# Kernel tuning notes

Measured on AMD Instinct MI355X. Metric: run time of the kernel, lower is better.

The kernel has to match this reference:

```python
import jax, jax.numpy as jnp
import numpy as np

H = 12          # num_heads
LENS_T = 64     # template tokens
LENS_S = 256    # search tokens
KEEP = int(0.7 * LENS_S)  # 179 kept search tokens


def _ln(x, s, b):
    mu = jnp.mean(x, axis=-1, keepdims=True)
    var = jnp.mean(jnp.square(x - mu), axis=-1, keepdims=True)
    return (x - mu) / jnp.sqrt(var + 1e-5) * s + b


def setup_inputs() -> dict:
    key = jax.random.key(0)
    ks = jax.random.split(key, 8)
    B, C, Hh = 32, 768, 3072
    N = LENS_T + LENS_S
    w = lambda k, shape: jax.random.normal(k, shape, jnp.float32) * 0.02
    return {
        "x": jax.random.normal(ks[0], (B, N, C), jnp.float32),
        "global_index_t": jnp.tile(jnp.arange(LENS_T, dtype=jnp.int32), (B, 1)),
        "global_index_s": jnp.tile(jnp.arange(LENS_S, dtype=jnp.int32), (B, 1)),
        "norm1_s": jnp.ones((C,), jnp.float32), "norm1_b": jnp.zeros((C,), jnp.float32),
        "qkv_w": w(ks[1], (C, 3 * C)), "qkv_b": jnp.zeros((3 * C,), jnp.float32),
        "proj_w": w(ks[2], (C, C)), "proj_b": jnp.zeros((C,), jnp.float32),
        "norm2_s": jnp.ones((C,), jnp.float32), "norm2_b": jnp.zeros((C,), jnp.float32),
        "fc1_w": w(ks[3], (C, Hh)), "fc1_b": jnp.zeros((Hh,), jnp.float32),
        "fc2_w": w(ks[4], (Hh, C)), "fc2_b": jnp.zeros((C,), jnp.float32),
        "gcn_w": w(ks[5], (C, C)), "gcn_b": jnp.zeros((C,), jnp.float32),
        "norm3_s": jnp.ones((C,), jnp.float32), "norm3_b": jnp.zeros((C,), jnp.float32),
    }


def reference(x, global_index_t, global_index_s,
              norm1_s, norm1_b, qkv_w, qkv_b, proj_w, proj_b,
              norm2_s, norm2_b, fc1_w, fc1_b, fc2_w, fc2_b,
              gcn_w, gcn_b, norm3_s, norm3_b):
    B, N, C = x.shape
    hd = C // H
    scale = hd ** -0.5

    # --- attention (attn weights explicitly materialized) ---
    h = _ln(x, norm1_s, norm1_b)
    qkv = (h @ qkv_w + qkv_b).reshape(B, N, 3, H, hd).transpose(2, 0, 3, 1, 4)
    q, k, v = qkv[0], qkv[1], qkv[2]                      # [B,H,N,hd]
    attn = jax.nn.softmax(jnp.einsum('bhqd,bhkd->bhqk', q, k) * scale, axis=-1)
    xa = jnp.einsum('bhqk,bhkd->bhqd', attn, v).transpose(0, 2, 1, 3).reshape(B, N, C)
    xa = xa @ proj_w + proj_b
    x = x + xa

    # --- MLP ---
    x_res = x
    h2 = _ln(x, norm2_s, norm2_b)
    h2 = jax.nn.gelu(h2 @ fc1_w + fc1_b, approximate=False) @ fc2_w + fc2_b
    x = x_res + h2

    # --- GCN using template<->search attention as adjacency ---
    # adjacency = [[0, w_ts], [w_ts^T, 0]]; exploit block sparsity instead of
    # materializing the dense [B,N,N] matrix.
    w_ts = jnp.sum(attn[:, :, :LENS_T, LENS_T:], axis=1) / H   # [B,T,S]
    w_ts = jax.nn.softmax(w_ts, axis=2)
    support = x @ gcn_w + gcn_b
    out_t = jnp.einsum('bts,bsd->btd', w_ts, support[:, LENS_T:])   # top block
    out_s = jnp.einsum('bts,btd->bsd', w_ts, support[:, :LENS_T])   # bottom block
    x = jnp.concatenate([out_t, out_s], axis=1)
    x = x + _ln(x, norm3_s, norm3_b)

    # --- top-k token pruning on search tokens ---
    score_s = jnp.mean(attn[:, :, :LENS_T, LENS_T:], axis=(1, 2))   # [B,S]
    order = jnp.argsort(-score_s, axis=1)
    keep_indices = order[:, :KEEP]
    removed_index_s = order[:, KEEP:]
    gs_new = jnp.take_along_axis(global_index_s, keep_indices, axis=1)
    idx = jnp.concatenate([global_index_t.astype(jnp.int32), keep_indices + LENS_T], axis=1)
    x = jnp.take_along_axis(x, jnp.broadcast_to(idx[..., None], (B, idx.shape[1], C)), axis=1)
    return (x, global_index_t, gs_new, removed_index_s, attn)
```

## Files before the change

### kernel.cpp

```cpp
#include <hip/hip_runtime.h>
#include <math.h>

#define NKEEP 179
#define NREM  77
#define NOUT_ROWS 243

typedef __bf16 bf16x8 __attribute__((ext_vector_type(8)));
typedef float f32x4 __attribute__((ext_vector_type(4)));

__device__ __forceinline__ unsigned short f2bf(float f) {
  unsigned u = __builtin_bit_cast(unsigned, f);
  u = (u + 0x7FFFu + ((u >> 16) & 1u)) >> 16;
  return (unsigned short)u;
}

__device__ __forceinline__ void gload_lds16(const void* g, void* l) {
  __builtin_amdgcn_global_load_lds((const __attribute__((address_space(1))) void*)g,
                                   (__attribute__((address_space(3))) void*)l,
                                   16, 0, 0);
}

template<int RESID, int OUTMODE>
__global__ __launch_bounds__(256)
void ln_kernel(const float* __restrict__ in, const float* __restrict__ gs,
               const float* __restrict__ gb, void* __restrict__ outp,
               void* __restrict__ outp2) {
  int row = blockIdx.x;
  const float* p = in + (size_t)row * 768;
  int tid = threadIdx.x;
  float v0 = p[tid], v1 = p[tid + 256], v2 = p[tid + 512];
  __shared__ double rs[256], rq[256];
  double d0 = v0, d1 = v1, d2 = v2;
  rs[tid] = d0 + d1 + d2;
  rq[tid] = d0 * d0 + d1 * d1 + d2 * d2;
  __syncthreads();
  for (int st = 128; st > 0; st >>= 1) {
    if (tid < st) { rs[tid] += rs[tid + st]; rq[tid] += rq[tid + st]; }
    __syncthreads();
  }
  double mu  = rs[0] * (1.0 / 768.0);
  double var = rq[0] * (1.0 / 768.0) - mu * mu;
  float rstd = (float)rsqrt(var + 1e-5);
  float muf = (float)mu;
  float y0 = (v0 - muf) * rstd * gs[tid]       + gb[tid];
  float y1 = (v1 - muf) * rstd * gs[tid + 256] + gb[tid + 256];
  float y2 = (v2 - muf) * rstd * gs[tid + 512] + gb[tid + 512];
  if (RESID) { y0 += v0; y1 += v1; y2 += v2; }
  if (OUTMODE == 0 || OUTMODE == 2) {
    float* o = (float*)outp + (size_t)row * 768;
    o[tid] = y0; o[tid + 256] = y1; o[tid + 512] = y2;
  }
  if (OUTMODE == 1) {
    unsigned short* o = (unsigned short*)outp + (size_t)row * 768;
    o[tid] = f2bf(y0); o[tid + 256] = f2bf(y1); o[tid + 512] = f2bf(y2);
  }
  if (OUTMODE == 2) {
    unsigned short* o = (unsigned short*)outp2 + (size_t)row * 768;
    o[tid] = f2bf(y0); o[tid + 256] = f2bf(y1); o[tid + 512] = f2bf(y2);
  }
}

__global__ __launch_bounds__(256)
void wtrans_kernel(const float* __restrict__ W, unsigned short* __restrict__ Wt,
                   int K, int N) {
  __shared__ float t[32][33];
  int n0 = blockIdx.x * 32, k0 = blockIdx.y * 32;
  int tid = threadIdx.x;
#pragma unroll
  for (int p = 0; p < 4; p++) {
    int idx = tid + p * 256;
    int r = idx >> 5, c = idx & 31;
    t[r][c] = W[(size_t)(k0 + r) * N + n0 + c];
  }
  __syncthreads();
#pragma unroll
  for (int p = 0; p < 4; p++) {
    int idx = tid + p * 256;
    int r = idx >> 5, c = idx & 31;
    Wt[(size_t)(n0 + r) * K + k0 + c] = f2bf(t[c][r]);
  }
}

template<int ACT, int RES, int OUTBF>
__global__ __launch_bounds__(256)
void gemm_bf16_kernel(const unsigned short* __restrict__ A,
                      const unsigned short* __restrict__ Bt,
                      const float* __restrict__ bias, const float* __restrict__ res,
                      void* __restrict__ outp, int M, int K, int N) {
  __shared__ unsigned short Al[128 * 64];
  __shared__ unsigned short Bl[128 * 64];
  int tid = threadIdx.x;
  int lane = tid & 63, wid = tid >> 6;
  int wr = wid >> 1, wc = wid & 1;
  int bm0 = blockIdx.x * 128, bn0 = blockIdx.y * 128;

  int r8 = lane >> 3;
  int csw = lane & 7;
  int csrc = csw ^ r8;

  const unsigned short* Abase = A + (size_t)bm0 * K + (size_t)csrc * 8;
  const unsigned short* Bbase = Bt + (size_t)bn0 * K + (size_t)csrc * 8;

  f32x4 acc[4][4] = {};

  int mrow = lane & 15;
  int kch = lane >> 4;
  int key = mrow & 7;

  for (int k0 = 0; k0 < K; k0 += 64) {
#pragma unroll
    for (int i = 0; i < 4; i++) {
      int rr = wid * 32 + i * 8;
      gload_lds16(Abase + (size_t)(rr + r8) * K + k0, Al + rr * 64);
      gload_lds16(Bbase + (size_t)(rr + r8) * K + k0, Bl + rr * 64);
    }
    __syncthreads();
#pragma unroll
    for (int ks = 0; ks < 2; ks++) {
      bf16x8 af[4], bfr[4];
#pragma unroll
      for (int f = 0; f < 4; f++) {
        int ra = wr * 64 + f * 16 + mrow;
        int ca = (ks * 4 + kch) ^ key;
        af[f] = *reinterpret_cast<const bf16x8*>(&Al[ra * 64 + ca * 8]);
        int rb = wc * 64 + f * 16 + mrow;
        bfr[f] = *reinterpret_cast<const bf16x8*>(&Bl[rb * 64 + ca * 8]);
      }
#pragma unroll
      for (int fm = 0; fm < 4; fm++)
#pragma unroll
        for (int fn = 0; fn < 4; fn++)
          acc[fm][fn] = __builtin_amdgcn_mfma_f32_16x16x32_bf16(
              af[fm], bfr[fn], acc[fm][fn], 0, 0, 0);
    }
    __syncthreads();
  }
#pragma unroll
  for (int fm = 0; fm < 4; fm++) {
#pragma unroll
    for (int j = 0; j < 4; j++) {
      int row = bm0 + wr * 64 + fm * 16 + (lane >> 4) * 4 + j;
#pragma unroll
      for (int fn = 0; fn < 4; fn++) {
        int col = bn0 + wc * 64 + fn * 16 + (lane & 15);
        float c = acc[fm][fn][j] + bias[col];
        if (ACT == 1) c = 0.5f * c * (1.0f + erff(c * 0.70710678118654752f));
        if (RES) c += res[(size_t)row * N + col];
        if (OUTBF) ((unsigned short*)outp)[(size_t)row * N + col] = f2bf(c);
        else       ((float*)outp)[(size_t)row * N + col] = c;
      }
    }
  }
}

__global__ __launch_bounds__(256)
void gemm_qkv_bf16_kernel(const unsigned short* __restrict__ A,
                          const unsigned short* __restrict__ Bt,
                          const float* __restrict__ bias,
                          float* __restrict__ Qb, float* __restrict__ Vb) {
  __shared__ unsigned short Al[128 * 64];
  __shared__ unsigned short Bl[128 * 64];
  const int K = 768;
  int tid = threadIdx.x;
  int lane = tid & 63, wid = tid >> 6;
  int wr = wid >> 1, wc = wid & 1;
  int by = blockIdx.y;
  int colbase = (by < 6) ? by * 128 : (by - 6) * 128 + 1536;
  int bm0 = blockIdx.x * 128;

  int r8 = lane >> 3;
  int csw = lane & 7;
  int csrc = csw ^ r8;

  const unsigned short* Abase = A + (size_t)bm0 * K + (size_t)csrc * 8;
  const unsigned short* Bbase = Bt + (size_t)colbase * K + (size_t)csrc * 8;

  f32x4 acc[4][4] = {};
  int mrow = lane & 15;
  int kch = lane >> 4;
  int key = mrow & 7;

  for (int k0 = 0; k0 < K; k0 += 64) {
#pragma unroll
    for (int i = 0; i < 4; i++) {
      int rr = wid * 32 + i * 8;
      gload_lds16(Abase + (size_t)(rr + r8) * K + k0, Al + rr * 64);
      gload_lds16(Bbase + (size_t)(rr + r8) * K + k0, Bl + rr * 64);
    }
    __syncthreads();
#pragma unroll
    for (int ks = 0; ks < 2; ks++) {
      bf16x8 af[4], bfr[4];
#pragma unroll
      for (int f = 0; f < 4; f++) {
        int ra = wr * 64 + f * 16 + mrow;
        int ca = (ks * 4 + kch) ^ key;
        af[f] = *reinterpret_cast<const bf16x8*>(&Al[ra * 64 + ca * 8]);
        int rb = wc * 64 + f * 16 + mrow;
        bfr[f] = *reinterpret_cast<const bf16x8*>(&Bl[rb * 64 + ca * 8]);
      }
#pragma unroll
      for (int fm = 0; fm < 4; fm++)
#pragma unroll
        for (int fn = 0; fn < 4; fn++)
          acc[fm][fn] = __builtin_amdgcn_mfma_f32_16x16x32_bf16(
              af[fm], bfr[fn], acc[fm][fn], 0, 0, 0);
    }
    __syncthreads();
  }
#pragma unroll
  for (int fm = 0; fm < 4; fm++) {
#pragma unroll
    for (int j = 0; j < 4; j++) {
      int row = bm0 + wr * 64 + fm * 16 + (lane >> 4) * 4 + j;
      int b = row / 320, nr = row - b * 320;
#pragma unroll
      for (int fn = 0; fn < 4; fn++) {
        int col = colbase + wc * 64 + fn * 16 + (lane & 15);
        int sel = col / 768;
        int rem = col - sel * 768;
        int h = rem >> 6, d = rem & 63;
        float* dstb = (sel == 0) ? Qb : Vb;
        dstb[(((size_t)(b * 12 + h) * 320 + nr) << 6) + d] = acc[fm][fn][j] + bias[col];
      }
    }
  }
}

template<int ROWMAP>
__global__ __launch_bounds__(256)
void gemm_prec_kernel(const float* __restrict__ A, const float* __restrict__ W,
                      const float* __restrict__ bias, int colOff,
                      float* __restrict__ Dst) {
  __shared__ float AsT[32][68];
  __shared__ float Bs[32][68];
  int tid = threadIdx.x;
  int tx = tid & 15, ty = tid >> 4;
  int bm0 = blockIdx.x * 64, bn0 = blockIdx.y * 64;

  int arow[2];
#pragma unroll
  for (int q = 0; q < 2; q++) {
    int idx = tid + q * 256;
    int m = bm0 + (idx >> 3);
    arow[q] = ROWMAP ? ((m >> 6) * 320 + (m & 63)) : m;
  }
  const float* Wbase = W + colOff + bn0;

  double master[4][4] = {};
  for (int k0 = 0; k0 < 768; k0 += 32) {
    float4 av[2], bv[2];
#pragma unroll
    for (int q = 0; q < 2; q++) {
      int idx = tid + q * 256;
      av[q] = *(const float4*)(A + (size_t)arow[q] * 768 + k0 + (idx & 7) * 4);
      int br = idx >> 4, bc4 = idx & 15;
      bv[q] = *(const float4*)(Wbase + (size_t)(k0 + br) * 2304 + bc4 * 4);
    }
    __syncthreads();
#pragma unroll
    for (int q = 0; q < 2; q++) {
      int idx = tid + q * 256;
      int r = idx >> 3, kc8 = idx & 7;
      AsT[kc8 * 4 + 0][r] = av[q].x;
      AsT[kc8 * 4 + 1][r] = av[q].y;
      AsT[kc8 * 4 + 2][r] = av[q].z;
      AsT[kc8 * 4 + 3][r] = av[q].w;
      *(float4*)&Bs[idx >> 4][(idx & 15) * 4] = bv[q];
    }
    __syncthreads();
#pragma unroll
    for (int half = 0; half < 2; half++) {
      float chunk[4][4] = {};
#pragma unroll
      for (int kk = 0; kk < 16; kk++) {
        int kkk = half * 16 + kk;
        float a[4], bb[4];
        *(float4*)a  = *(const float4*)&AsT[kkk][ty * 4];
        *(float4*)bb = *(const float4*)&Bs[kkk][tx * 4];
#pragma unroll
        for (int i = 0; i < 4; i++)
#pragma unroll
          for (int j = 0; j < 4; j++) chunk[i][j] = fmaf(a[i], bb[j], chunk[i][j]);
      }
#pragma unroll
      for (int i = 0; i < 4; i++)
#pragma unroll
        for (int j = 0; j < 4; j++) master[i][j] += (double)chunk[i][j];
    }
    __syncthreads();
  }
  int n0 = bn0 + tx * 4;
  int h = n0 >> 6, d = n0 & 63;
#pragma unroll
  for (int i = 0; i < 4; i++) {
    int m = bm0 + ty * 4 + i;
    int b, nr;
    if (ROWMAP) { b = m >> 6; nr = m & 63; }
    else        { b = m / 320; nr = m - b * 320; }
    float* dst = Dst + (((size_t)(b * 12 + h) * 320 + nr) << 6) + d;
    float4 v;
    v.x = (float)master[i][0] + bias[colOff + n0];
    v.y = (float)master[i][1] + bias[colOff + n0 + 1];
    v.z = (float)master[i][2] + bias[colOff + n0 + 2];
    v.w = (float)master[i][3] + bias[colOff + n0 + 3];
    *(float4*)dst = v;
  }
}

__global__ __launch_bounds__(256)
void attn_fused_kernel(const float* __restrict__ Qb, const float* __restrict__ Kb,
                       const float* __restrict__ Vb, float* __restrict__ attn,
                       unsigned short* __restrict__ xa) {
  __shared__ float Qs[64][68];
  __shared__ float Ks[64][68];
  float (*Ps)[68] = Qs;
  int bid = blockIdx.x;
  int qt = bid / 384, bh = bid % 384;
  int h = bh % 12, b = bh / 12;
  int q0 = qt * 64;
  int t = threadIdx.x;
  int tx = t & 15, ty = t >> 4;
  const float* Qg = Qb + (((size_t)bh * 320 + q0) << 6);
  const float* Kg = Kb + (((size_t)bh * 320) << 6);
  const float* Vg = Vb + (((size_t)bh * 320) << 6);
  float* attn_bh = attn + ((size_t)bh * 320 + q0) * 320;

  {
    int r = t >> 2, c = (t & 3) * 16;
    const float* src = Qg + (r << 6) + c;
#pragma unroll
    for (int i = 0; i < 4; i++)
      *(float4*)&Qs[r][c + i * 4] = *(const float4*)(src + i * 4);
  }

  float s[4][20];
  float mrow[4] = {-1e30f, -1e30f, -1e30f, -1e30f};

#pragma unroll
  for (int kc = 0; kc < 5; ++kc) {
    __syncthreads();
    {
      int r = t >> 2, c = (t & 3) * 16;
      const float* src = Kg + ((size_t)(kc * 64 + r) << 6) + c;
#pragma unroll
      for (int i = 0; i < 4; i++)
        *(float4*)&Ks[r][c + i * 4] = *(const float4*)(src + i * 4);
    }
    __syncthreads();
    float acc[4][4] = {};
#pragma unroll 4
    for (int d0 = 0; d0 < 64; d0 += 4) {
      float4 qv[4], kv[4];
#pragma unroll
      for (int i = 0; i < 4; i++) qv[i] = *(const float4*)&Qs[ty * 4 + i][d0];
#pragma unroll
      for (int j = 0; j < 4; j++) kv[j] = *(const float4*)&Ks[tx * 4 + j][d0];
#pragma unroll
      for (int i = 0; i < 4; i++)
#pragma unroll
        for (int j = 0; j < 4; j++) {
          acc[i][j] = fmaf(qv[i].x, kv[j].x, acc[i][j]);
          acc[i][j] = fmaf(qv[i].y, kv[j].y, acc[i][j]);
          acc[i][j] = fmaf(qv[i].z, kv[j].z, acc[i][j]);
          acc[i][j] = fmaf(qv[i].w, kv[j].w, acc[i][j]);
        }
    }
#pragma unroll
    for (int i = 0; i < 4; i++) {
      float sx = acc[i][0] * 0.125f, sy = acc[i][1] * 0.125f;
      float sz = acc[i][2] * 0.125f, sw = acc[i][3] * 0.125f;
      mrow[i] = fmaxf(mrow[i], fmaxf(fmaxf(sx, sy), fmaxf(sz, sw)));
      s[i][kc * 4 + 0] = sx; s[i][kc * 4 + 1] = sy;
      s[i][kc * 4 + 2] = sz; s[i][kc * 4 + 3] = sw;
    }
  }
#pragma unroll
  for (int i = 0; i < 4; i++) {
    mrow[i] = fmaxf(mrow[i], __shfl_xor(mrow[i], 1, 16));
    mrow[i] = fmaxf(mrow[i], __shfl_xor(mrow[i], 2, 16));
    mrow[i] = fmaxf(mrow[i], __shfl_xor(mrow[i], 4, 16));
    mrow[i] = fmaxf(mrow[i], __shfl_xor(mrow[i], 8, 16));
  }

  double lsum[4] = {0.0, 0.0, 0.0, 0.0};
#pragma unroll
  for (int i = 0; i < 4; i++)
#pragma unroll
    for (int c = 0; c < 20; c++) {
      float e = expf(s[i][c] - mrow[i]);
      s[i][c] = e;
      lsum[i] += (double)e;
    }
#pragma unroll
  for (int i = 0; i < 4; i++) {
    lsum[i] += __shfl_xor(lsum[i], 1, 16);
    lsum[i] += __shfl_xor(lsum[i], 2, 16);
    lsum[i] += __shfl_xor(lsum[i], 4, 16);
    lsum[i] += __shfl_xor(lsum[i], 8, 16);
  }
  float inv[4];
#pragma unroll
  for (int i = 0; i < 4; i++) inv[i] = (float)(1.0 / lsum[i]);

#pragma unroll
  for (int i = 0; i < 4; i++)
#pragma unroll
    for (int kc = 0; kc < 5; kc++) {
      float4 sv;
      sv.x = s[i][kc * 4 + 0] * inv[i];
      sv.y = s[i][kc * 4 + 1] * inv[i];
      sv.z = s[i][kc * 4 + 2] * inv[i];
      sv.w = s[i][kc * 4 + 3] * inv[i];
      *(float4*)&attn_bh[(size_t)(ty * 4 + i) * 320 + kc * 64 + tx * 4] = sv;
    }

  float acc2[4][4] = {};
  for (int kc = 0; kc < 5; ++kc) {
    __syncthreads();
    {
      int r = t >> 2, c = (t & 3) * 16;
      const float* src = Vg + ((size_t)(kc * 64 + r) << 6) + c;
#pragma unroll
      for (int i = 0; i < 4; i++)
        *(float4*)&Ks[r][c + i * 4] = *(const float4*)(src + i * 4);
    }
#pragma unroll
    for (int i = 0; i < 4; i++) {
      float4 sv;
      sv.x = s[i][kc * 4 + 0] * inv[i];
      sv.y = s[i][kc * 4 + 1] * inv[i];
      sv.z = s[i][kc * 4 + 2] * inv[i];
      sv.w = s[i][kc * 4 + 3] * inv[i];
      *(float4*)&Ps[ty * 4 + i][tx * 4] = sv;
    }
    __syncthreads();
#pragma unroll 4
    for (int kk4 = 0; kk4 < 16; ++kk4) {
      float4 pv[4], vv[4];
#pragma unroll
      for (int i = 0; i < 4; i++)
        pv[i] = *(const float4*)&Ps[ty * 4 + i][kk4 * 4];
#pragma unroll
      for (int l = 0; l < 4; l++) vv[l] = *(const float4*)&Ks[kk4 * 4 + l][tx * 4];
#pragma unroll
      for (int i = 0; i < 4; i++) {
        acc2[i][0] = fmaf(pv[i].x, vv[0].x, acc2[i][0]);
        acc2[i][1] = fmaf(pv[i].x, vv[0].y, acc2[i][1]);
        acc2[i][2] = fmaf(pv[i].x, vv[0].z, acc2[i][2]);
        acc2[i][3] = fmaf(pv[i].x, vv[0].w, acc2[i][3]);
        acc2[i][0] = fmaf(pv[i].y, vv[1].x, acc2[i][0]);
        acc2[i][1] = fmaf(pv[i].y, vv[1].y, acc2[i][1]);
        acc2[i][2] = fmaf(pv[i].y, vv[1].z, acc2[i][2]);
        acc2[i][3] = fmaf(pv[i].y, vv[1].w, acc2[i][3]);
        acc2[i][0] = fmaf(pv[i].z, vv[2].x, acc2[i][0]);
        acc2[i][1] = fmaf(pv[i].z, vv[2].y, acc2[i][1]);
        acc2[i][2] = fmaf(pv[i].z, vv[2].z, acc2[i][2]);
        acc2[i][3] = fmaf(pv[i].z, vv[2].w, acc2[i][3]);
        acc2[i][0] = fmaf(pv[i].w, vv[3].x, acc2[i][0]);
        acc2[i][1] = fmaf(pv[i].w, vv[3].y, acc2[i][1]);
        acc2[i][2] = fmaf(pv[i].w, vv[3].z, acc2[i][2]);
        acc2[i][3] = fmaf(pv[i].w, vv[3].w, acc2[i][3]);
      }
    }
  }
#pragma unroll
  for (int i = 0; i < 4; i++) {
    unsigned short* dst = xa + (size_t)(b * 320 + q0 + ty * 4 + i) * 768 + h * 64 + tx * 4;
    uint2 pk;
    pk.x = (unsigned)f2bf(acc2[i][0]) | ((unsigned)f2bf(acc2[i][1]) << 16);
    pk.y = (unsigned)f2bf(acc2[i][2]) | ((unsigned)f2bf(acc2[i][3]) << 16);
    *(uint2*)dst = pk;
  }
}

__global__ __launch_bounds__(256)
void wts_kernel(const float* __restrict__ attn, float* __restrict__ wts) {
  int bid = blockIdx.x;
  int tt = bid & 63, b = bid >> 6;
  int s = threadIdx.x;
  float acc = 0.0f;
  const float* base = attn + (((size_t)(b * 12)) * 320 + tt) * 320 + 64 + s;
#pragma unroll
  for (int h = 0; h < 12; h++) acc += base[(size_t)h * 320 * 320];
  acc *= (1.0f / 12.0f);
  __shared__ float red[256];
  red[s] = acc; __syncthreads();
  for (int st = 128; st > 0; st >>= 1) {
    if (s < st) red[s] = fmaxf(red[s], red[s + st]);
    __syncthreads();
  }
  float m = red[0]; __syncthreads();
  float e = expf(acc - m);
  red[s] = e; __syncthreads();
  for (int st = 128; st > 0; st >>= 1) {
    if (s < st) red[s] += red[s + st];
    __syncthreads();
  }
  wts[(size_t)bid * 256 + s] = e / red[0];
}

__global__ __launch_bounds__(256)
void out_t_kernel(const float* __restrict__ wts, const float* __restrict__ sup,
                  float* __restrict__ x3) {
  int idx = blockIdx.x * 256 + threadIdx.x;
  int c = idx % 768;
  int tt = (idx / 768) % 64;
  int b = idx / (768 * 64);
  const float* wrow = wts + (size_t)(b * 64 + tt) * 256;
  const float* sp = sup + ((size_t)(b * 320 + 64)) * 768 + c;
  float acc = 0.0f;
  for (int s = 0; s < 256; s++) acc = fmaf(wrow[s], sp[(size_t)s * 768], acc);
  x3[((size_t)(b * 320 + tt)) * 768 + c] = acc;
}

__global__ __launch_bounds__(256)
void out_s_kernel(const float* __restrict__ wts, const float* __restrict__ sup,
                  float* __restrict__ x3) {
  int idx = blockIdx.x * 256 + threadIdx.x;
  int c = idx % 768;
  int s = (idx / 768) % 256;
  int b = idx / (768 * 256);
  const float* wp = wts + (size_t)(b * 64) * 256 + s;
  const float* sp = sup + ((size_t)(b * 320)) * 768 + c;
  float acc = 0.0f;
#pragma unroll 4
  for (int tt = 0; tt < 64; tt++) acc = fmaf(wp[(size_t)tt * 256], sp[(size_t)tt * 768], acc);
  x3[((size_t)(b * 320 + 64 + s)) * 768 + c] = acc;
}

__global__ __launch_bounds__(256)
void score_part_kernel(const float* __restrict__ attn, double* __restrict__ part) {
  int h = blockIdx.x, b = blockIdx.y;
  int s = threadIdx.x;
  const float* base = attn + (((size_t)(b * 12 + h)) * 320) * 320 + 64 + s;
  double acc = 0.0;
  for (int tt = 0; tt < 64; tt++) acc += (double)base[(size_t)tt * 320];
  part[((size_t)(b * 12 + h)) * 256 + s] = acc;
}

__global__ __launch_bounds__(256)
void score_final_kernel(const double* __restrict__ part, const int* __restrict__ git,
                        const int* __restrict__ gis, int* __restrict__ order_ws,
                        float* __restrict__ out_git, float* __restrict__ out_gs,
                        float* __restrict__ out_rm) {
  int b = blockIdx.x, s = threadIdx.x;
  double acc = 0.0;
#pragma unroll
  for (int h = 0; h < 12; h++) acc += part[((size_t)(b * 12 + h)) * 256 + s];
  __shared__ double sc[256];
  __shared__ int ord[256];
  sc[s] = acc;
  __syncthreads();
  double my = sc[s];
  int r = 0;
  for (int i = 0; i < 256; i++) {
    double si = sc[i];
    r += (si > my) || (si == my && i < s);
  }
  ord[r] = s;
  __syncthreads();
  int o = ord[s];
  order_ws[b * 256 + s] = o;
  if (s < NKEEP) out_gs[b * NKEEP + s] = (float)gis[b * 256 + o];
  else           out_rm[b * NREM + (s - NKEEP)] = (float)o;
  if (s < 64)    out_git[b * 64 + s] = (float)git[b * 64 + s];
}

__global__ __launch_bounds__(256)
void gather_kernel(const float* __restrict__ x3, const int* __restrict__ git,
                   const int* __restrict__ order_ws, float* __restrict__ out) {
  int bid = blockIdx.x;
  int j = bid % NOUT_ROWS, b = bid / NOUT_ROWS;
  int src = (j < 64) ? git[b * 64 + j] : (order_ws[b * 256 + (j - 64)] + 64);
  const float* p = x3 + ((size_t)(b * 320 + src)) * 768;
  float* o = out + ((size_t)(b * NOUT_ROWS + j)) * 768;
  int tid = threadIdx.x;
  o[tid] = p[tid]; o[tid + 256] = p[tid + 256]; o[tid + 512] = p[tid + 512];
}

extern "C" void kernel_launch(void* const* d_in, const int* in_sizes, int n_in,
                              void* d_out, int out_size, void* d_ws, size_t ws_size,
                              hipStream_t stream) {
  (void)in_sizes; (void)n_in; (void)out_size; (void)ws_size;
  const float* x      = (const float*)d_in[0];
  const int*   git    = (const int*)d_in[1];
  const int*   gis    = (const int*)d_in[2];
  const float* n1s    = (const float*)d_in[3];
  const float* n1b    = (const float*)d_in[4];
  const float* qkv_w  = (const float*)d_in[5];
  const float* qkv_b  = (const float*)d_in[6];
  const float* proj_w = (const float*)d_in[7];
  const float* proj_b = (const float*)d_in[8];
  const float* n2s    = (const float*)d_in[9];
  const float* n2b    = (const float*)d_in[10];
  const float* fc1_w  = (const float*)d_in[11];
  const float* fc1_b  = (const float*)d_in[12];
  const float* fc2_w  = (const float*)d_in[13];
  const float* fc2_b  = (const float*)d_in[14];
  const float* gcn_w  = (const float*)d_in[15];
  const float* gcn_b  = (const float*)d_in[16];
  const float* n3s    = (const float*)d_in[17];
  const float* n3b    = (const float*)d_in[18];

  float* out     = (float*)d_out;
  float* out_x   = out;
  float* out_git = out + 5971968;
  float* out_gs  = out + 5974016;
  float* out_rm  = out + 5979744;
  float* attn    = out + 5982208;

  float* w      = (float*)d_ws;
  float* bufA   = w;
  float* bufB   = w + 7864320;
  float* bufBIG = w + 15728640;
  float* Qbuf = bufBIG;
  float* Kbuf = bufBIG + 7864320;
  float* Vbuf = bufBIG + 15728640;
  unsigned short* ln1_bf = (unsigned short*)(bufBIG + 23592960);
  unsigned short* f1_bf = (unsigned short*)bufBIG;
  unsigned short* x2_bf = (unsigned short*)(bufBIG + 15728640);
  float* x3 = bufBIG + 19660800;
  unsigned short* wbf = (unsigned short*)(bufBIG + 27525120);
  unsigned short* proj_wt = wbf;
  unsigned short* fc1_wt  = wbf + 589824;
  unsigned short* fc2_wt  = fc1_wt + 2359296;
  unsigned short* gcn_wt  = fc2_wt + 2359296;
  unsigned short* qkv_wt  = gcn_wt + 589824;
  unsigned short* xa_bf = (unsigned short*)bufA;
  unsigned short* h2_bf = (unsigned short*)bufA;
  float* wts    = bufBIG + 31457280;
  int*   order_ws = (int*)(wts + 524288);
  double* partd  = (double*)(wts + 524288 + 8192);

  const int M = 10240;

  wtrans_kernel<<<dim3(24, 24), dim3(256), 0, stream>>>(proj_w, proj_wt, 768, 768);
  wtrans_kernel<<<dim3(96, 24), dim3(256), 0, stream>>>(fc1_w, fc1_wt, 768, 3072);
  wtrans_kernel<<<dim3(24, 96), dim3(256), 0, stream>>>(fc2_w, fc2_wt, 3072, 768);
  wtrans_kernel<<<dim3(24, 24), dim3(256), 0, stream>>>(gcn_w, gcn_wt, 768, 768);
  wtrans_kernel<<<dim3(72, 24), dim3(256), 0, stream>>>(qkv_w, qkv_wt, 768, 2304);

  ln_kernel<0, 2><<<dim3(M), dim3(256), 0, stream>>>(x, n1s, n1b, bufA, ln1_bf);
  gemm_qkv_bf16_kernel<<<dim3(80, 12), dim3(256), 0, stream>>>(
      ln1_bf, qkv_wt, qkv_b, Qbuf, Vbuf);
  gemm_prec_kernel<0><<<dim3(160, 12), dim3(256), 0, stream>>>(
      bufA, qkv_w, qkv_b, 768, Kbuf);
  gemm_prec_kernel<1><<<dim3(32, 12), dim3(256), 0, stream>>>(
      bufA, qkv_w, qkv_b, 0, Qbuf);
  attn_fused_kernel<<<dim3(1920), dim3(256), 0, stream>>>(
      Qbuf, Kbuf, Vbuf, attn, xa_bf);
  gemm_bf16_kernel<0, 1, 0><<<dim3(M / 128, 768 / 128), dim3(256), 0, stream>>>(
      xa_bf, proj_wt, proj_b, x, bufB, M, 768, 768);
  ln_kernel<0, 1><<<dim3(M), dim3(256), 0, stream>>>(bufB, n2s, n2b, h2_bf, nullptr);
  gemm_bf16_kernel<1, 0, 1><<<dim3(M / 128, 3072 / 128), dim3(256), 0, stream>>>(
      h2_bf, fc1_wt, fc1_b, nullptr, f1_bf, M, 768, 3072);
  gemm_bf16_kernel<0, 1, 1><<<dim3(M / 128, 768 / 128), dim3(256), 0, stream>>>(
      f1_bf, fc2_wt, fc2_b, bufB, x2_bf, M, 3072, 768);
  wts_kernel<<<dim3(32 * 64), dim3(256), 0, stream>>>(attn, wts);
  gemm_bf16_kernel<0, 0, 0><<<dim3(M / 128, 768 / 128), dim3(256), 0, stream>>>(
      x2_bf, gcn_wt, gcn_b, nullptr, bufA, M, 768, 768);
  out_t_kernel<<<dim3(32 * 64 * 768 / 256), dim3(256), 0, stream>>>(wts, bufA, x3);
  out_s_kernel<<<dim3(32 * 256 * 768 / 256), dim3(256), 0, stream>>>(wts, bufA, x3);
  ln_kernel<1, 0><<<dim3(M), dim3(256), 0, stream>>>(x3, n3s, n3b, x3, nullptr);
  score_part_kernel<<<dim3(12, 32), dim3(256), 0, stream>>>(attn, partd);
  score_final_kernel<<<dim3(32), dim3(256), 0, stream>>>(partd, git, gis, order_ws,
                                                         out_git, out_gs, out_rm);
  gather_kernel<<<dim3(32 * NOUT_ROWS), dim3(256), 0, stream>>>(x3, git,
                                                                order_ws, out_x);
}
```

Before: 1.015 ms.

## Narrow N-tile for 768-wide GEMMs and prefetch registers in fp32 precision GEMM

The bf16 GEMM gains a template tile-width parameter, and the 768-output GEMMs (proj, fc2, gcn) now use 128x64 tiles. This doubles the block count (80x6 becomes 80x12 = 960 blocks) so more CUs stay busy, at the cost of less reuse of A per block. The fp32/double-accumulate GEMM now prefetches the next K slice into registers while computing the current one. It also stores A row-major with padding instead of transposed, so A values are read as scalar LDS loads rather than float4.

```diff
diff --git a/kernel.cpp b/kernel.cpp
--- a/kernel.cpp
+++ b/kernel.cpp
@@ -81,18 +81,19 @@
   }
 }
 
-template<int ACT, int RES, int OUTBF>
+template<int ACT, int RES, int OUTBF, int BN>
 __global__ __launch_bounds__(256)
 void gemm_bf16_kernel(const unsigned short* __restrict__ A,
                       const unsigned short* __restrict__ Bt,
                       const float* __restrict__ bias, const float* __restrict__ res,
                       void* __restrict__ outp, int M, int K, int N) {
+  constexpr int NF = BN / 32;
   __shared__ unsigned short Al[128 * 64];
-  __shared__ unsigned short Bl[128 * 64];
+  __shared__ unsigned short Bl[BN * 64];
   int tid = threadIdx.x;
   int lane = tid & 63, wid = tid >> 6;
   int wr = wid >> 1, wc = wid & 1;
-  int bm0 = blockIdx.x * 128, bn0 = blockIdx.y * 128;
+  int bm0 = blockIdx.x * 128, bn0 = blockIdx.y * BN;
 
   int r8 = lane >> 3;
   int csw = lane & 7;
@@ -101,7 +102,7 @@
   const unsigned short* Abase = A + (size_t)bm0 * K + (size_t)csrc * 8;
   const unsigned short* Bbase = Bt + (size_t)bn0 * K + (size_t)csrc * 8;
 
-  f32x4 acc[4][4] = {};
+  f32x4 acc[4][NF] = {};
 
   int mrow = lane & 15;
   int kch = lane >> 4;
@@ -112,24 +113,32 @@
     for (int i = 0; i < 4; i++) {
       int rr = wid * 32 + i * 8;
       gload_lds16(Abase + (size_t)(rr + r8) * K + k0, Al + rr * 64);
+    }
+#pragma unroll
+    for (int i = 0; i < NF; i++) {
+      int rr = wid * (BN / 4) + i * 8;
       gload_lds16(Bbase + (size_t)(rr + r8) * K + k0, Bl + rr * 64);
     }
     __syncthreads();
 #pragma unroll
     for (int ks = 0; ks < 2; ks++) {
-      bf16x8 af[4], bfr[4];
+      bf16x8 af[4], bfr[NF];
 #pragma unroll
       for (int f = 0; f < 4; f++) {
         int ra = wr * 64 + f * 16 + mrow;
         int ca = (ks * 4 + kch) ^ key;
         af[f] = *reinterpret_cast<const bf16x8*>(&Al[ra * 64 + ca * 8]);
-        int rb = wc * 64 + f * 16 + mrow;
+      }
+#pragma unroll
+      for (int f = 0; f < NF; f++) {
+        int ca = (ks * 4 + kch) ^ key;
+        int rb = wc * (BN / 2) + f * 16 + mrow;
         bfr[f] = *reinterpret_cast<const bf16x8*>(&Bl[rb * 64 + ca * 8]);
       }
 #pragma unroll
       for (int fm = 0; fm < 4; fm++)
 #pragma unroll
-        for (int fn = 0; fn < 4; fn++)
+        for (int fn = 0; fn < NF; fn++)
           acc[fm][fn] = __builtin_amdgcn_mfma_f32_16x16x32_bf16(
               af[fm], bfr[fn], acc[fm][fn], 0, 0, 0);
     }
@@ -141,8 +150,8 @@
     for (int j = 0; j < 4; j++) {
       int row = bm0 + wr * 64 + fm * 16 + (lane >> 4) * 4 + j;
 #pragma unroll
-      for (int fn = 0; fn < 4; fn++) {
-        int col = bn0 + wc * 64 + fn * 16 + (lane & 15);
+      for (int fn = 0; fn < NF; fn++) {
+        int col = bn0 + wc * (BN / 2) + fn * 16 + (lane & 15);
         float c = acc[fm][fn][j] + bias[col];
         if (ACT == 1) c = 0.5f * c * (1.0f + erff(c * 0.70710678118654752f));
         if (RES) c += res[(size_t)row * N + col];
@@ -232,7 +241,7 @@
 void gemm_prec_kernel(const float* __restrict__ A, const float* __restrict__ W,
                       const float* __restrict__ bias, int colOff,
                       float* __restrict__ Dst) {
-  __shared__ float AsT[32][68];
+  __shared__ float As[64][36];
   __shared__ float Bs[32][68];
   int tid = threadIdx.x;
   int tx = tid & 15, ty = tid >> 4;
@@ -247,28 +256,33 @@
   }
   const float* Wbase = W + colOff + bn0;
 
+  float4 av[2], bv[2];
+#pragma unroll
+  for (int q = 0; q < 2; q++) {
+    int idx = tid + q * 256;
+    av[q] = *(const float4*)(A + (size_t)arow[q] * 768 + (idx & 7) * 4);
+    bv[q] = *(const float4*)(Wbase + (size_t)(idx >> 4) * 2304 + (idx & 15) * 4);
+  }
+
   double master[4][4] = {};
   for (int k0 = 0; k0 < 768; k0 += 32) {
-    float4 av[2], bv[2];
+    __syncthreads();
 #pragma unroll
     for (int q = 0; q < 2; q++) {
       int idx = tid + q * 256;
-      av[q] = *(const float4*)(A + (size_t)arow[q] * 768 + k0 + (idx & 7) * 4);
-      int br = idx >> 4, bc4 = idx & 15;
-      bv[q] = *(const float4*)(Wbase + (size_t)(k0 + br) * 2304 + bc4 * 4);
-    }
-    __syncthreads();
-#pragma unroll
-    for (int q = 0; q < 2; q++) {
-      int idx = tid + q * 256;
-      int r = idx >> 3, kc8 = idx & 7;
-      AsT[kc8 * 4 + 0][r] = av[q].x;
-      AsT[kc8 * 4 + 1][r] = av[q].y;
-      AsT[kc8 * 4 + 2][r] = av[q].z;
-      AsT[kc8 * 4 + 3][r] = av[q].w;
+      *(float4*)&As[idx >> 3][(idx & 7) * 4] = av[q];
       *(float4*)&Bs[idx >> 4][(idx & 15) * 4] = bv[q];
     }
     __syncthreads();
+    if (k0 + 32 < 768) {
+      int kn = k0 + 32;
+#pragma unroll
+      for (int q = 0; q < 2; q++) {
+        int idx = tid + q * 256;
+        av[q] = *(const float4*)(A + (size_t)arow[q] * 768 + kn + (idx & 7) * 4);
+        bv[q] = *(const float4*)(Wbase + (size_t)(kn + (idx >> 4)) * 2304 + (idx & 15) * 4);
+      }
+    }
 #pragma unroll
     for (int half = 0; half < 2; half++) {
       float chunk[4][4] = {};
@@ -276,9 +290,10 @@
       for (int kk = 0; kk < 16; kk++) {
         int kkk = half * 16 + kk;
         float a[4], bb[4];
-        *(float4*)a  = *(const float4*)&AsT[kkk][ty * 4];
         *(float4*)bb = *(const float4*)&Bs[kkk][tx * 4];
 #pragma unroll
+        for (int i = 0; i < 4; i++) a[i] = As[ty * 4 + i][kkk];
+#pragma unroll
         for (int i = 0; i < 4; i++)
 #pragma unroll
           for (int j = 0; j < 4; j++) chunk[i][j] = fmaf(a[i], bb[j], chunk[i][j]);
@@ -288,7 +303,6 @@
 #pragma unroll
         for (int j = 0; j < 4; j++) master[i][j] += (double)chunk[i][j];
     }
-    __syncthreads();
   }
   int n0 = bn0 + tx * 4;
   int h = n0 >> 6, d = n0 & 63;
@@ -650,15 +664,15 @@
       bufA, qkv_w, qkv_b, 0, Qbuf);
   attn_fused_kernel<<<dim3(1920), dim3(256), 0, stream>>>(
       Qbuf, Kbuf, Vbuf, attn, xa_bf);
-  gemm_bf16_kernel<0, 1, 0><<<dim3(M / 128, 768 / 128), dim3(256), 0, stream>>>(
+  gemm_bf16_kernel<0, 1, 0, 64><<<dim3(M / 128, 768 / 64), dim3(256), 0, stream>>>(
       xa_bf, proj_wt, proj_b, x, bufB, M, 768, 768);
   ln_kernel<0, 1><<<dim3(M), dim3(256), 0, stream>>>(bufB, n2s, n2b, h2_bf, nullptr);
-  gemm_bf16_kernel<1, 0, 1><<<dim3(M / 128, 3072 / 128), dim3(256), 0, stream>>>(
+  gemm_bf16_kernel<1, 0, 1, 128><<<dim3(M / 128, 3072 / 128), dim3(256), 0, stream>>>(
       h2_bf, fc1_wt, fc1_b, nullptr, f1_bf, M, 768, 3072);
-  gemm_bf16_kernel<0, 1, 1><<<dim3(M / 128, 768 / 128), dim3(256), 0, stream>>>(
+  gemm_bf16_kernel<0, 1, 1, 64><<<dim3(M / 128, 768 / 64), dim3(256), 0, stream>>>(
       f1_bf, fc2_wt, fc2_b, bufB, x2_bf, M, 3072, 768);
   wts_kernel<<<dim3(32 * 64), dim3(256), 0, stream>>>(attn, wts);
-  gemm_bf16_kernel<0, 0, 0><<<dim3(M / 128, 768 / 128), dim3(256), 0, stream>>>(
+  gemm_bf16_kernel<0, 0, 0, 64><<<dim3(M / 128, 768 / 64), dim3(256), 0, stream>>>(
       x2_bf, gcn_wt, gcn_b, nullptr, bufA, M, 768, 768);
   out_t_kernel<<<dim3(32 * 64 * 768 / 256), dim3(256), 0, stream>>>(wts, bufA, x3);
   out_s_kernel<<<dim3(32 * 256 * 768 / 256), dim3(256), 0, stream>>>(wts, bufA, x3);
```

New measurement: 1.101 ms. 8.5% more time.
